# Kernel tuning notes

Hardware: AMD Instinct MI355X
Metric: run time of the kernel (lower is better)

The kernel has to match this reference:

```python
import jax, jax.numpy as jnp
import numpy as np

B, S, H, I, E = 4, 4096, 1024, 4096, 4
VOCAB = 32000


def setup_inputs() -> dict:
    key = jax.random.key(0)
    k1, k2, k3, k4, k5 = jax.random.split(key, 5)
    scale = 1.0 / np.sqrt(H)
    return {
        "hidden_states": jax.random.normal(k1, (B, S, H), dtype=jnp.float32),
        "gate_proj": jax.random.normal(k2, (E, H, I), dtype=jnp.float32) * scale,
        "up_proj": jax.random.normal(k3, (E, H, I), dtype=jnp.float32) * scale,
        "down_proj": jax.random.normal(k4, (E, I, H), dtype=jnp.float32) * (1.0 / np.sqrt(I)),
        "token_ids": jax.random.randint(k5, (B, S), 0, VOCAB, dtype=jnp.int64),
    }


def reference(hidden_states, gate_proj, up_proj, down_proj, token_ids):
    # hidden_states: [B, S, H]; token_ids: [B, S]
    num_experts = gate_proj.shape[0]
    expert_ids = token_ids % num_experts  # [B, S]
    out = jnp.zeros_like(hidden_states)
    for e in range(num_experts):  # small fixed expert loop
        gate = jax.nn.silu(jnp.einsum("bsh,hi->bsi", hidden_states, gate_proj[e]))
        up = jnp.einsum("bsh,hi->bsi", hidden_states, up_proj[e])
        y = jnp.einsum("bsi,ih->bsh", gate * up, down_proj[e])
        out = jnp.where((expert_ids == e)[..., None], y, out)
    return out
```

## Files before the change

### kernel.cpp

```cpp
#include <hip/hip_runtime.h>

#define TOK    16384
#define HD     1024
#define ID     4096
#define NE     4
#define MAXMT  131
#define MAXMT2 67
#define NT32   (HD / 32)

typedef __attribute__((ext_vector_type(4))) float f32x4;
typedef __attribute__((ext_vector_type(8))) short bf16x8;
typedef unsigned int u32;

static __device__ __forceinline__ unsigned short f2bf(float f) {
  unsigned u = __float_as_uint(f);
  u += 0x7FFFu + ((u >> 16) & 1u);
  return (unsigned short)(u >> 16);
}

static __device__ __forceinline__ void gl16(const void* g, void* l) {
  __builtin_amdgcn_global_load_lds((const __attribute__((address_space(1))) u32*)g,
                                   (__attribute__((address_space(3))) u32*)l, 16, 0, 0);
}

static __device__ __forceinline__ void barx() {
  asm volatile("" ::: "memory");
  __builtin_amdgcn_s_barrier();
  asm volatile("" ::: "memory");
}

__global__ void k_route0(const int* __restrict__ ids, int* __restrict__ meta) {
  __shared__ int cnt[4];
  int t = threadIdx.x;
  if (t < 4) cnt[t] = 0;
  __syncthreads();
  int l0 = 0, l1 = 0, l2 = 0, l3 = 0;
  for (int i = t; i < TOK; i += 256) {
    int e = ids[i] & 3;
    l0 += (e == 0); l1 += (e == 1); l2 += (e == 2); l3 += (e == 3);
  }
  atomicAdd(&cnt[0], l0); atomicAdd(&cnt[1], l1);
  atomicAdd(&cnt[2], l2); atomicAdd(&cnt[3], l3);
  __syncthreads();
  if (t == 0) {
    int o = 0;
    for (int e = 0; e < 4; ++e) { meta[e] = o; meta[8 + e] = o; o += cnt[e]; }
    meta[4] = o;
  }
}

__global__ void k_route1(const int* __restrict__ ids, int* __restrict__ meta,
                         int* __restrict__ perm) {
  int i = blockIdx.x * 256 + threadIdx.x;
  if (i < TOK) {
    int e = ids[i] & 3;
    int s = atomicAdd(&meta[8 + e], 1);
    perm[s] = i;
  }
}

__global__ void k_conv(const float* __restrict__ s, unsigned short* __restrict__ d, int n8) {
  int i = blockIdx.x * blockDim.x + threadIdx.x;
  int st = gridDim.x * blockDim.x;
  for (; i < n8; i += st) {
    const f32x4* p = (const f32x4*)(s + ((size_t)i << 3));
    f32x4 a = p[0], b = p[1];
    union { unsigned short u[8]; uint4 q; } o;
    o.u[0] = f2bf(a.x); o.u[1] = f2bf(a.y); o.u[2] = f2bf(a.z); o.u[3] = f2bf(a.w);
    o.u[4] = f2bf(b.x); o.u[5] = f2bf(b.y); o.u[6] = f2bf(b.z); o.u[7] = f2bf(b.w);
    *(uint4*)(d + ((size_t)i << 3)) = o.q;
  }
}

__global__ void k_tr12(const float* __restrict__ gw, const float* __restrict__ uw,
                       const float* __restrict__ dw, unsigned short* __restrict__ gT,
                       unsigned short* __restrict__ uT, unsigned short* __restrict__ dT) {
  __shared__ float tile[64][65];
  int z = blockIdx.y;
  const float* s; unsigned short* d; int R, C, lg;
  if (z < 8) {
    R = HD; C = ID; lg = 6;
    int m = z & 3;
    if (z < 4) { s = gw + (size_t)m * R * C; d = gT + (size_t)m * R * C; }
    else       { s = uw + (size_t)m * R * C; d = uT + (size_t)m * R * C; }
  } else {
    R = ID; C = HD; lg = 4;
    int m = z - 8;
    s = dw + (size_t)m * R * C; d = dT + (size_t)m * R * C;
  }
  int bx = blockIdx.x;
  int tx = bx & ((1 << lg) - 1), ty = bx >> lg;
  int r0 = ty << 6, c0 = tx << 6;
  int t = threadIdx.x;
  int lr = t >> 4, lc = (t & 15) << 2;
  #pragma unroll
  for (int it = 0; it < 4; ++it) {
    int r = lr + (it << 4);
    f32x4 v = *(const f32x4*)(s + (size_t)(r0 + r) * C + c0 + lc);
    tile[r][lc] = v.x; tile[r][lc + 1] = v.y; tile[r][lc + 2] = v.z; tile[r][lc + 3] = v.w;
  }
  __syncthreads();
  int c = t >> 2, rb = (t & 3) << 4;
  union { unsigned short u[16]; uint4 q[2]; } o;
  #pragma unroll
  for (int j = 0; j < 16; ++j) o.u[j] = f2bf(tile[rb + j][c]);
  uint4* dp = (uint4*)(d + (size_t)(c0 + c) * R + r0 + rb);
  dp[0] = o.q[0]; dp[1] = o.q[1];
}

#define MFMA16 __builtin_amdgcn_mfma_f32_16x16x32_bf16
#define BASE4(T) (((T) & 3) * 32768)

#define RD1(T, FA, FB) { const char* bb = smem + BASE4(T); \
  _Pragma("unroll") for (int m = 0; m < 4; ++m) FA[m] = *(const bf16x8*)(bb + offA0[m]); \
  _Pragma("unroll") for (int n = 0; n < 4; ++n) FB[n] = *(const bf16x8*)(bb + offB[n]); }

#define RD2(T, FA) { const char* bb = smem + BASE4(T); \
  _Pragma("unroll") for (int m = 0; m < 4; ++m) FA[m] = *(const bf16x8*)(bb + offA1[m]); }

#define STG(T, H) { int tt = (T) < NT32 ? (T) : NT32 - 1; int ko = tt * 32; \
  char* bb = smem + BASE4(T); \
  gl16(srcA[H] + ko, bb + dA[H]); gl16(srcB[H] + ko, bb + dB[H]); }

#define CLUSTER(FA, FB, MH, NW) \
  barx(); \
  asm volatile("s_waitcnt lgkmcnt(" #NW ")" ::: "memory"); \
  __builtin_amdgcn_sched_barrier(0); \
  __builtin_amdgcn_s_setprio(1); \
  { _Pragma("unroll") for (int m = 0; m < 4; ++m) \
    _Pragma("unroll") for (int n = 0; n < 4; ++n) \
      acc[(MH) * 4 + m][n] = MFMA16(FA[m], FB[n], acc[(MH) * 4 + m][n], 0, 0, 0); } \
  __builtin_amdgcn_s_setprio(0)

__global__ __launch_bounds__(512, 2) void k_gemm1(
    const unsigned short* __restrict__ hid,
    const unsigned short* __restrict__ gT,
    const unsigned short* __restrict__ uT,
    const int* __restrict__ meta,
    const int* __restrict__ perm,
    unsigned short* __restrict__ act) {
  extern __shared__ __align__(16) char smem[];
  int offs[5];
  #pragma unroll
  for (int i = 0; i < 5; ++i) offs[i] = meta[i];
  int bid = blockIdx.x;
  int logical = (bid & 7) * (MAXMT2 * 32 / 8) + (bid >> 3);
  int mt = logical >> 5;
  int ny = logical & 31;
  int e = -1, mloc = 0, base = 0;
  #pragma unroll
  for (int ee = 0; ee < 4; ++ee) {
    int tiles = (offs[ee + 1] - offs[ee] + 255) >> 8;
    if (e < 0 && mt < base + tiles) { e = ee; mloc = mt - base; }
    base += tiles;
  }
  if (e < 0) return;
  int slot0 = offs[e] + (mloc << 8);
  int send = offs[e + 1];
  int tid = threadIdx.x, lane = tid & 63, wid = tid >> 6;
  int n0 = ny << 7;

  int sslot = (tid & 3) ^ ((tid >> 3) & 3);
  int ke = sslot << 3;
  const unsigned short* srcA[2];
  const unsigned short* srcB[2];
  int dA[2], dB[2];
  const unsigned short* gb = gT + (size_t)e * ID * HD;
  const unsigned short* ub = uT + (size_t)e * ID * HD;
  #pragma unroll
  for (int j = 0; j < 2; ++j) {
    int r = (tid >> 2) + j * 128;
    int slot = slot0 + r;
    int pr = perm[slot < send ? slot : slot0];
    srcA[j] = hid + (size_t)pr * HD + ke;
    dA[j] = (tid << 4) + j * 8192;
    int sB = r >> 4;
    int grow = n0 + ((sB >> 1) << 4) + (r & 15);
    srcB[j] = ((sB & 1) ? ub : gb) + (size_t)grow * HD + ke;
    dB[j] = 16384 + (tid << 4) + j * 8192;
  }

  int wm = wid >> 2, wn = wid & 3;
  int r16 = lane & 15, kg = lane >> 4;
  int offA0[4], offA1[4], offB[4];
  #pragma unroll
  for (int m = 0; m < 4; ++m) {
    int r0 = wm * 128 + m * 16 + r16;
    offA0[m] = r0 * 64 + ((kg << 4) ^ (((r0 >> 1) & 3) << 4));
    int r1 = r0 + 64;
    offA1[m] = r1 * 64 + ((kg << 4) ^ (((r1 >> 1) & 3) << 4));
  }
  #pragma unroll
  for (int n = 0; n < 4; ++n) {
    int rb = wn * 64 + n * 16 + r16;
    offB[n] = 16384 + rb * 64 + ((kg << 4) ^ (((rb >> 1) & 3) << 4));
  }

  f32x4 acc[8][4];
  #pragma unroll
  for (int m = 0; m < 8; ++m)
    #pragma unroll
    for (int n = 0; n < 4; ++n) acc[m][n] = (f32x4){0.f, 0.f, 0.f, 0.f};
  bf16x8 faX[4], faY[4], fbE[4], fbO[4];

  STG(0, 0); STG(0, 1);
  STG(1, 0); STG(1, 1);
  STG(2, 0);
  asm volatile("s_waitcnt vmcnt(6)" ::: "memory");
  barx();
  RD1(0, faX, fbE);

  #pragma unroll 1
  for (int i = 0; i < NT32 / 2; ++i) {
    int te = 2 * i, to = 2 * i + 1;
    RD2(te, faY);
    STG(te + 2, 1);
    asm volatile("s_waitcnt vmcnt(4)" ::: "memory");
    CLUSTER(faX, fbE, 0, 4);
    RD1(to, faX, fbO);
    STG(te + 3, 0);
    CLUSTER(faY, fbE, 1, 8);
    RD2(to, faY);
    STG(te + 3, 1);
    asm volatile("s_waitcnt vmcnt(4)" ::: "memory");
    CLUSTER(faX, fbO, 0, 4);
    RD1(te + 2, faX, fbE);
    STG(te + 4, 0);
    CLUSTER(faY, fbO, 1, 8);
  }
  asm volatile("s_waitcnt vmcnt(0) lgkmcnt(0)" ::: "memory");

  #pragma unroll
  for (int mf = 0; mf < 8; ++mf) {
    int lr = wm * 128 + mf * 16 + kg * 4;
    #pragma unroll
    for (int np = 0; np < 2; ++np) {
      int col = n0 + (2 * wn + np) * 16 + r16;
      #pragma unroll
      for (int r = 0; r < 4; ++r) {
        int slot = slot0 + lr + r;
        if (slot < send) {
          float g = acc[mf][2 * np][r];
          float u = acc[mf][2 * np + 1][r];
          float y = (g / (1.f + __expf(-g))) * u;
          act[(size_t)slot * ID + col] = f2bf(y);
        }
      }
    }
  }
}

__global__ __launch_bounds__(256, 2) void k_gemm2(
    const unsigned short* __restrict__ act,
    const unsigned short* __restrict__ dT,
    const int* __restrict__ meta,
    const int* __restrict__ perm,
    float* __restrict__ out) {
  __shared__ unsigned short As[128 * 64];
  __shared__ unsigned short Bs[128 * 64];
  int offs[5];
  #pragma unroll
  for (int i = 0; i < 5; ++i) offs[i] = meta[i];
  int bid = blockIdx.x;
  int logical = (bid & 7) * (MAXMT * 8 / 8) + (bid >> 3);
  int mt = logical >> 3;
  int nyy = logical & 7;
  int e = -1, mloc = 0, base = 0;
  #pragma unroll
  for (int ee = 0; ee < 4; ++ee) {
    int tiles = (offs[ee + 1] - offs[ee] + 127) >> 7;
    if (e < 0 && mt < base + tiles) { e = ee; mloc = mt - base; }
    base += tiles;
  }
  if (e < 0) return;
  int slot0 = offs[e] + (mloc << 7);
  int send = offs[e + 1];
  int tid = threadIdx.x;
  int n0 = nyy << 7;
  const unsigned short* dbase = dT + (size_t)e * HD * ID;
  const unsigned short* ap[4];
  const unsigned short* bp[4];
  int wofs[4];
  #pragma unroll
  for (int it = 0; it < 4; ++it) {
    int b = (tid << 4) + (it << 12);
    int row = b >> 7;
    int kob = b & 127;
    int slot = slot0 + row;
    int s2 = slot < send ? slot : slot0;
    ap[it] = act + (size_t)s2 * ID + (kob >> 1);
    bp[it] = dbase + (size_t)(n0 + row) * ID + (kob >> 1);
    wofs[it] = row * 64 + ((kob ^ ((row & 7) << 4)) >> 1);
  }
  int lane = tid & 63, wid = tid >> 6;
  int wm = wid >> 1, wn = wid & 1;
  int r16 = lane & 15, kg = lane >> 4;
  f32x4 zero = {0.f, 0.f, 0.f, 0.f};
  f32x4 acc[4][4];
  #pragma unroll
  for (int m = 0; m < 4; ++m)
    #pragma unroll
    for (int n = 0; n < 4; ++n) acc[m][n] = zero;

  bf16x8 sa[4], sb[4];
  #pragma unroll
  for (int it = 0; it < 4; ++it) {
    sa[it] = *(const bf16x8*)(ap[it]);
    sb[it] = *(const bf16x8*)(bp[it]);
  }
  for (int kt = 0; kt < ID / 64; ++kt) {
    __syncthreads();
    #pragma unroll
    for (int it = 0; it < 4; ++it) {
      *(bf16x8*)(As + wofs[it]) = sa[it];
      *(bf16x8*)(Bs + wofs[it]) = sb[it];
    }
    __syncthreads();
    if (kt < ID / 64 - 1) {
      int ko = (kt + 1) << 6;
      #pragma unroll
      for (int it = 0; it < 4; ++it) {
        sa[it] = *(const bf16x8*)(ap[it] + ko);
        sb[it] = *(const bf16x8*)(bp[it] + ko);
      }
    }
    #pragma unroll
    for (int kk = 0; kk < 2; ++kk) {
      bf16x8 fa[4], fb[4];
      #pragma unroll
      for (int m = 0; m < 4; ++m) {
        int row = (wm << 6) + (m << 4) + r16;
        int kob = (kk << 6) + (kg << 4);
        fa[m] = *(const bf16x8*)(As + row * 64 + ((kob ^ ((row & 7) << 4)) >> 1));
      }
      #pragma unroll
      for (int n = 0; n < 4; ++n) {
        int row = (wn << 6) + (n << 4) + r16;
        int kob = (kk << 6) + (kg << 4);
        fb[n] = *(const bf16x8*)(Bs + row * 64 + ((kob ^ ((row & 7) << 4)) >> 1));
      }
      #pragma unroll
      for (int m = 0; m < 4; ++m)
        #pragma unroll
        for (int n = 0; n < 4; ++n)
          acc[m][n] = __builtin_amdgcn_mfma_f32_16x16x32_bf16(fa[m], fb[n], acc[m][n], 0, 0, 0);
    }
  }
  #pragma unroll
  for (int m = 0; m < 4; ++m) {
    int lr = (wm << 6) + (m << 4) + (kg << 2);
    int pr4[4];
    #pragma unroll
    for (int r = 0; r < 4; ++r) {
      int slot = slot0 + lr + r;
      pr4[r] = slot < send ? perm[slot] : -1;
    }
    #pragma unroll
    for (int n = 0; n < 4; ++n) {
      int col = n0 + (wn << 6) + (n << 4) + r16;
      #pragma unroll
      for (int r = 0; r < 4; ++r) {
        if (pr4[r] >= 0) out[(size_t)pr4[r] * HD + col] = acc[m][n][r];
      }
    }
  }
}

extern "C" void kernel_launch(void* const* d_in, const int* in_sizes, int n_in,
                              void* d_out, int out_size, void* d_ws, size_t ws_size,
                              hipStream_t stream) {
  const float* hs = (const float*)d_in[0];
  const float* gw = (const float*)d_in[1];
  const float* uw = (const float*)d_in[2];
  const float* dw = (const float*)d_in[3];
  const int* ids = (const int*)d_in[4];
  float* out = (float*)d_out;

  char* w = (char*)d_ws;
  size_t o = 0;
  int* meta = (int*)(w + o); o += 64;
  int* perm = (int*)(w + o); o += (size_t)TOK * 4;
  o = (o + 255) & ~(size_t)255;
  unsigned short* hid = (unsigned short*)(w + o); o += (size_t)TOK * HD * 2;
  unsigned short* gT  = (unsigned short*)(w + o); o += (size_t)NE * ID * HD * 2;
  unsigned short* uT  = (unsigned short*)(w + o); o += (size_t)NE * ID * HD * 2;
  unsigned short* dT  = (unsigned short*)(w + o); o += (size_t)NE * ID * HD * 2;
  unsigned short* actb = (unsigned short*)(w + o); o += (size_t)TOK * ID * 2;

  hipFuncSetAttribute((const void*)k_gemm1,
                      hipFuncAttributeMaxDynamicSharedMemorySize, 131072);

  hipLaunchKernelGGL(k_route0, dim3(1), dim3(256), 0, stream, ids, meta);
  hipLaunchKernelGGL(k_route1, dim3(TOK / 256), dim3(256), 0, stream, ids, meta, perm);
  hipLaunchKernelGGL(k_conv, dim3(2048), dim3(256), 0, stream, hs, hid, TOK * HD / 8);
  hipLaunchKernelGGL(k_tr12, dim3(1024, 12), dim3(256), 0, stream, gw, uw, dw, gT, uT, dT);
  hipLaunchKernelGGL(k_gemm1, dim3(MAXMT2 * 32), dim3(512), 131072, stream,
                     hid, gT, uT, meta, perm, actb);
  hipLaunchKernelGGL(k_gemm2, dim3(MAXMT * 8), dim3(256), 0, stream,
                     actb, dT, meta, perm, out);
}
```

Baseline: 694.0 us.

## Replace pipelined 256-row gemm1 with simpler 128-row single-buffer kernels

Drops the hand-scheduled 4-stage pipelined gemm1 (512 threads, 256x128 tiles, 128KB dynamic LDS) and replaces it with a simple 256-thread kernel on 128-row tiles. The new kernel loads A, gate and up tiles straight to LDS each k-step, waits on vmcnt(0), then runs separate gate and up accumulators. gemm2 is also moved to direct global-to-LDS loads with a swizzled layout, replacing its register-staged copies, and its occupancy hint is raised to 3. The aim is simpler code and higher occupancy, at the cost of losing load/compute overlap and halving M reuse in gemm1.

```diff
diff --git a/kernel.cpp b/kernel.cpp
--- a/kernel.cpp
+++ b/kernel.cpp
@@ -5,8 +5,6 @@
 #define ID     4096
 #define NE     4
 #define MAXMT  131
-#define MAXMT2 67
-#define NT32   (HD / 32)
 
 typedef __attribute__((ext_vector_type(4))) float f32x4;
 typedef __attribute__((ext_vector_type(8))) short bf16x8;
@@ -109,139 +107,119 @@
 }
 
 #define MFMA16 __builtin_amdgcn_mfma_f32_16x16x32_bf16
-#define BASE4(T) (((T) & 3) * 32768)
-
-#define RD1(T, FA, FB) { const char* bb = smem + BASE4(T); \
-  _Pragma("unroll") for (int m = 0; m < 4; ++m) FA[m] = *(const bf16x8*)(bb + offA0[m]); \
-  _Pragma("unroll") for (int n = 0; n < 4; ++n) FB[n] = *(const bf16x8*)(bb + offB[n]); }
-
-#define RD2(T, FA) { const char* bb = smem + BASE4(T); \
-  _Pragma("unroll") for (int m = 0; m < 4; ++m) FA[m] = *(const bf16x8*)(bb + offA1[m]); }
-
-#define STG(T, H) { int tt = (T) < NT32 ? (T) : NT32 - 1; int ko = tt * 32; \
-  char* bb = smem + BASE4(T); \
-  gl16(srcA[H] + ko, bb + dA[H]); gl16(srcB[H] + ko, bb + dB[H]); }
-
-#define CLUSTER(FA, FB, MH, NW) \
-  barx(); \
-  asm volatile("s_waitcnt lgkmcnt(" #NW ")" ::: "memory"); \
-  __builtin_amdgcn_sched_barrier(0); \
-  __builtin_amdgcn_s_setprio(1); \
-  { _Pragma("unroll") for (int m = 0; m < 4; ++m) \
-    _Pragma("unroll") for (int n = 0; n < 4; ++n) \
-      acc[(MH) * 4 + m][n] = MFMA16(FA[m], FB[n], acc[(MH) * 4 + m][n], 0, 0, 0); } \
-  __builtin_amdgcn_s_setprio(0)
-
-__global__ __launch_bounds__(512, 2) void k_gemm1(
+
+__global__ __launch_bounds__(256, 2) void k_gemm1(
     const unsigned short* __restrict__ hid,
     const unsigned short* __restrict__ gT,
     const unsigned short* __restrict__ uT,
     const int* __restrict__ meta,
     const int* __restrict__ perm,
     unsigned short* __restrict__ act) {
-  extern __shared__ __align__(16) char smem[];
+  __shared__ __align__(16) char smem[49152];
   int offs[5];
   #pragma unroll
   for (int i = 0; i < 5; ++i) offs[i] = meta[i];
   int bid = blockIdx.x;
-  int logical = (bid & 7) * (MAXMT2 * 32 / 8) + (bid >> 3);
+  int logical = (bid & 7) * (MAXMT * 32 / 8) + (bid >> 3);
   int mt = logical >> 5;
   int ny = logical & 31;
   int e = -1, mloc = 0, base = 0;
   #pragma unroll
   for (int ee = 0; ee < 4; ++ee) {
-    int tiles = (offs[ee + 1] - offs[ee] + 255) >> 8;
+    int tiles = (offs[ee + 1] - offs[ee] + 127) >> 7;
     if (e < 0 && mt < base + tiles) { e = ee; mloc = mt - base; }
     base += tiles;
   }
   if (e < 0) return;
-  int slot0 = offs[e] + (mloc << 8);
+  int slot0 = offs[e] + (mloc << 7);
   int send = offs[e + 1];
   int tid = threadIdx.x, lane = tid & 63, wid = tid >> 6;
   int n0 = ny << 7;
 
-  int sslot = (tid & 3) ^ ((tid >> 3) & 3);
-  int ke = sslot << 3;
-  const unsigned short* srcA[2];
-  const unsigned short* srcB[2];
-  int dA[2], dB[2];
   const unsigned short* gb = gT + (size_t)e * ID * HD;
   const unsigned short* ub = uT + (size_t)e * ID * HD;
-  #pragma unroll
-  for (int j = 0; j < 2; ++j) {
-    int r = (tid >> 2) + j * 128;
+  int rsub = tid >> 3;
+  int ks = tid & 7;
+  const unsigned short* srcA[4];
+  const unsigned short* srcG[4];
+  const unsigned short* srcU[4];
+  #pragma unroll
+  for (int j = 0; j < 4; ++j) {
+    int r = j * 32 + rsub;
+    int ko = (ks ^ (r & 7)) << 3;
     int slot = slot0 + r;
     int pr = perm[slot < send ? slot : slot0];
-    srcA[j] = hid + (size_t)pr * HD + ke;
-    dA[j] = (tid << 4) + j * 8192;
-    int sB = r >> 4;
-    int grow = n0 + ((sB >> 1) << 4) + (r & 15);
-    srcB[j] = ((sB & 1) ? ub : gb) + (size_t)grow * HD + ke;
-    dB[j] = 16384 + (tid << 4) + j * 8192;
-  }
-
-  int wm = wid >> 2, wn = wid & 3;
+    srcA[j] = hid + (size_t)pr * HD + ko;
+    srcG[j] = gb + (size_t)(n0 + r) * HD + ko;
+    srcU[j] = ub + (size_t)(n0 + r) * HD + ko;
+  }
+  int dstl = tid << 4;
+
+  int wm = wid >> 1, wn = wid & 1;
   int r16 = lane & 15, kg = lane >> 4;
-  int offA0[4], offA1[4], offB[4];
+  int offA[4], offG[4], offU[4];
   #pragma unroll
   for (int m = 0; m < 4; ++m) {
-    int r0 = wm * 128 + m * 16 + r16;
-    offA0[m] = r0 * 64 + ((kg << 4) ^ (((r0 >> 1) & 3) << 4));
-    int r1 = r0 + 64;
-    offA1[m] = r1 * 64 + ((kg << 4) ^ (((r1 >> 1) & 3) << 4));
+    int r = wm * 64 + m * 16 + r16;
+    offA[m] = r * 128 + ((kg ^ (r & 7)) << 4);
   }
   #pragma unroll
   for (int n = 0; n < 4; ++n) {
-    int rb = wn * 64 + n * 16 + r16;
-    offB[n] = 16384 + rb * 64 + ((kg << 4) ^ (((rb >> 1) & 3) << 4));
-  }
-
-  f32x4 acc[8][4];
-  #pragma unroll
-  for (int m = 0; m < 8; ++m)
-    #pragma unroll
-    for (int n = 0; n < 4; ++n) acc[m][n] = (f32x4){0.f, 0.f, 0.f, 0.f};
-  bf16x8 faX[4], faY[4], fbE[4], fbO[4];
-
-  STG(0, 0); STG(0, 1);
-  STG(1, 0); STG(1, 1);
-  STG(2, 0);
-  asm volatile("s_waitcnt vmcnt(6)" ::: "memory");
-  barx();
-  RD1(0, faX, fbE);
-
-  #pragma unroll 1
-  for (int i = 0; i < NT32 / 2; ++i) {
-    int te = 2 * i, to = 2 * i + 1;
-    RD2(te, faY);
-    STG(te + 2, 1);
-    asm volatile("s_waitcnt vmcnt(4)" ::: "memory");
-    CLUSTER(faX, fbE, 0, 4);
-    RD1(to, faX, fbO);
-    STG(te + 3, 0);
-    CLUSTER(faY, fbE, 1, 8);
-    RD2(to, faY);
-    STG(te + 3, 1);
-    asm volatile("s_waitcnt vmcnt(4)" ::: "memory");
-    CLUSTER(faX, fbO, 0, 4);
-    RD1(te + 2, faX, fbE);
-    STG(te + 4, 0);
-    CLUSTER(faY, fbO, 1, 8);
-  }
-  asm volatile("s_waitcnt vmcnt(0) lgkmcnt(0)" ::: "memory");
-
-  #pragma unroll
-  for (int mf = 0; mf < 8; ++mf) {
-    int lr = wm * 128 + mf * 16 + kg * 4;
-    #pragma unroll
-    for (int np = 0; np < 2; ++np) {
-      int col = n0 + (2 * wn + np) * 16 + r16;
+    int r = wn * 64 + n * 16 + r16;
+    int o = r * 128 + ((kg ^ (r & 7)) << 4);
+    offG[n] = 16384 + o;
+    offU[n] = 32768 + o;
+  }
+
+  f32x4 ag[4][4], au[4][4];
+  #pragma unroll
+  for (int m = 0; m < 4; ++m)
+    #pragma unroll
+    for (int n = 0; n < 4; ++n) { ag[m][n] = (f32x4){0,0,0,0}; au[m][n] = (f32x4){0,0,0,0}; }
+
+  for (int t = 0; t < HD / 64; ++t) {
+    barx();
+    int ko = t * 64;
+    #pragma unroll
+    for (int j = 0; j < 4; ++j) gl16(srcA[j] + ko, smem + j * 4096 + dstl);
+    #pragma unroll
+    for (int j = 0; j < 4; ++j) gl16(srcG[j] + ko, smem + 16384 + j * 4096 + dstl);
+    #pragma unroll
+    for (int j = 0; j < 4; ++j) gl16(srcU[j] + ko, smem + 32768 + j * 4096 + dstl);
+    asm volatile("s_waitcnt vmcnt(0)" ::: "memory");
+    barx();
+    #pragma unroll
+    for (int kk = 0; kk < 2; ++kk) {
+      bf16x8 fa[4], fg[4], fu[4];
+      #pragma unroll
+      for (int m = 0; m < 4; ++m) fa[m] = *(const bf16x8*)(smem + (offA[m] ^ (kk << 6)));
+      #pragma unroll
+      for (int n = 0; n < 4; ++n) {
+        fg[n] = *(const bf16x8*)(smem + (offG[n] ^ (kk << 6)));
+        fu[n] = *(const bf16x8*)(smem + (offU[n] ^ (kk << 6)));
+      }
+      #pragma unroll
+      for (int m = 0; m < 4; ++m)
+        #pragma unroll
+        for (int n = 0; n < 4; ++n) {
+          ag[m][n] = MFMA16(fa[m], fg[n], ag[m][n], 0, 0, 0);
+          au[m][n] = MFMA16(fa[m], fu[n], au[m][n], 0, 0, 0);
+        }
+    }
+  }
+
+  #pragma unroll
+  for (int m = 0; m < 4; ++m) {
+    int lr = (wm << 6) + (m << 4) + (kg << 2);
+    #pragma unroll
+    for (int n = 0; n < 4; ++n) {
+      int col = n0 + (wn << 6) + (n << 4) + r16;
       #pragma unroll
       for (int r = 0; r < 4; ++r) {
         int slot = slot0 + lr + r;
         if (slot < send) {
-          float g = acc[mf][2 * np][r];
-          float u = acc[mf][2 * np + 1][r];
+          float g = ag[m][n][r];
+          float u = au[m][n][r];
           float y = (g / (1.f + __expf(-g))) * u;
           act[(size_t)slot * ID + col] = f2bf(y);
         }
@@ -250,14 +228,13 @@
   }
 }
 
-__global__ __launch_bounds__(256, 2) void k_gemm2(
+__global__ __launch_bounds__(256, 3) void k_gemm2(
     const unsigned short* __restrict__ act,
     const unsigned short* __restrict__ dT,
     const int* __restrict__ meta,
     const int* __restrict__ perm,
     float* __restrict__ out) {
-  __shared__ unsigned short As[128 * 64];
-  __shared__ unsigned short Bs[128 * 64];
+  __shared__ __align__(16) char smem[32768];
   int offs[5];
   #pragma unroll
   for (int i = 0; i < 5; ++i) offs[i] = meta[i];
@@ -275,77 +252,69 @@
   if (e < 0) return;
   int slot0 = offs[e] + (mloc << 7);
   int send = offs[e + 1];
-  int tid = threadIdx.x;
+  int tid = threadIdx.x, lane = tid & 63, wid = tid >> 6;
   int n0 = nyy << 7;
   const unsigned short* dbase = dT + (size_t)e * HD * ID;
-  const unsigned short* ap[4];
-  const unsigned short* bp[4];
-  int wofs[4];
-  #pragma unroll
-  for (int it = 0; it < 4; ++it) {
-    int b = (tid << 4) + (it << 12);
-    int row = b >> 7;
-    int kob = b & 127;
-    int slot = slot0 + row;
+
+  int rsub = tid >> 3;
+  int ks = tid & 7;
+  const unsigned short* srcA[4];
+  const unsigned short* srcB[4];
+  #pragma unroll
+  for (int j = 0; j < 4; ++j) {
+    int r = j * 32 + rsub;
+    int ko = (ks ^ (r & 7)) << 3;
+    int slot = slot0 + r;
     int s2 = slot < send ? slot : slot0;
-    ap[it] = act + (size_t)s2 * ID + (kob >> 1);
-    bp[it] = dbase + (size_t)(n0 + row) * ID + (kob >> 1);
-    wofs[it] = row * 64 + ((kob ^ ((row & 7) << 4)) >> 1);
-  }
-  int lane = tid & 63, wid = tid >> 6;
+    srcA[j] = act + (size_t)s2 * ID + ko;
+    srcB[j] = dbase + (size_t)(n0 + r) * ID + ko;
+  }
+  int dstl = tid << 4;
+
   int wm = wid >> 1, wn = wid & 1;
   int r16 = lane & 15, kg = lane >> 4;
-  f32x4 zero = {0.f, 0.f, 0.f, 0.f};
+  int offA[4], offB[4];
+  #pragma unroll
+  for (int m = 0; m < 4; ++m) {
+    int r = wm * 64 + m * 16 + r16;
+    offA[m] = r * 128 + ((kg ^ (r & 7)) << 4);
+  }
+  #pragma unroll
+  for (int n = 0; n < 4; ++n) {
+    int r = wn * 64 + n * 16 + r16;
+    offB[n] = 16384 + r * 128 + ((kg ^ (r & 7)) << 4);
+  }
+
   f32x4 acc[4][4];
   #pragma unroll
   for (int m = 0; m < 4; ++m)
     #pragma unroll
-    for (int n = 0; n < 4; ++n) acc[m][n] = zero;
-
-  bf16x8 sa[4], sb[4];
-  #pragma unroll
-  for (int it = 0; it < 4; ++it) {
-    sa[it] = *(const bf16x8*)(ap[it]);
-    sb[it] = *(const bf16x8*)(bp[it]);
-  }
-  for (int kt = 0; kt < ID / 64; ++kt) {
-    __syncthreads();
-    #pragma unroll
-    for (int it = 0; it < 4; ++it) {
-      *(bf16x8*)(As + wofs[it]) = sa[it];
-      *(bf16x8*)(Bs + wofs[it]) = sb[it];
-    }
-    __syncthreads();
-    if (kt < ID / 64 - 1) {
-      int ko = (kt + 1) << 6;
-      #pragma unroll
-      for (int it = 0; it < 4; ++it) {
-        sa[it] = *(const bf16x8*)(ap[it] + ko);
-        sb[it] = *(const bf16x8*)(bp[it] + ko);
-      }
-    }
+    for (int n = 0; n < 4; ++n) acc[m][n] = (f32x4){0,0,0,0};
+
+  for (int t = 0; t < ID / 64; ++t) {
+    barx();
+    int ko = t * 64;
+    #pragma unroll
+    for (int j = 0; j < 4; ++j) gl16(srcA[j] + ko, smem + j * 4096 + dstl);
+    #pragma unroll
+    for (int j = 0; j < 4; ++j) gl16(srcB[j] + ko, smem + 16384 + j * 4096 + dstl);
+    asm volatile("s_waitcnt vmcnt(0)" ::: "memory");
+    barx();
     #pragma unroll
     for (int kk = 0; kk < 2; ++kk) {
       bf16x8 fa[4], fb[4];
       #pragma unroll
-      for (int m = 0; m < 4; ++m) {
-        int row = (wm << 6) + (m << 4) + r16;
-        int kob = (kk << 6) + (kg << 4);
-        fa[m] = *(const bf16x8*)(As + row * 64 + ((kob ^ ((row & 7) << 4)) >> 1));
-      }
-      #pragma unroll
-      for (int n = 0; n < 4; ++n) {
-        int row = (wn << 6) + (n << 4) + r16;
-        int kob = (kk << 6) + (kg << 4);
-        fb[n] = *(const bf16x8*)(Bs + row * 64 + ((kob ^ ((row & 7) << 4)) >> 1));
-      }
+      for (int m = 0; m < 4; ++m) fa[m] = *(const bf16x8*)(smem + (offA[m] ^ (kk << 6)));
+      #pragma unroll
+      for (int n = 0; n < 4; ++n) fb[n] = *(const bf16x8*)(smem + (offB[n] ^ (kk << 6)));
       #pragma unroll
       for (int m = 0; m < 4; ++m)
         #pragma unroll
         for (int n = 0; n < 4; ++n)
-          acc[m][n] = __builtin_amdgcn_mfma_f32_16x16x32_bf16(fa[m], fb[n], acc[m][n], 0, 0, 0);
-    }
-  }
+          acc[m][n] = MFMA16(fa[m], fb[n], acc[m][n], 0, 0, 0);
+    }
+  }
+
   #pragma unroll
   for (int m = 0; m < 4; ++m) {
     int lr = (wm << 6) + (m << 4) + (kg << 2);
@@ -387,14 +356,11 @@
   unsigned short* dT  = (unsigned short*)(w + o); o += (size_t)NE * ID * HD * 2;
   unsigned short* actb = (unsigned short*)(w + o); o += (size_t)TOK * ID * 2;
 
-  hipFuncSetAttribute((const void*)k_gemm1,
-                      hipFuncAttributeMaxDynamicSharedMemorySize, 131072);
-
   hipLaunchKernelGGL(k_route0, dim3(1), dim3(256), 0, stream, ids, meta);
   hipLaunchKernelGGL(k_route1, dim3(TOK / 256), dim3(256), 0, stream, ids, meta, perm);
   hipLaunchKernelGGL(k_conv, dim3(2048), dim3(256), 0, stream, hs, hid, TOK * HD / 8);
   hipLaunchKernelGGL(k_tr12, dim3(1024, 12), dim3(256), 0, stream, gw, uw, dw, gT, uT, dT);
-  hipLaunchKernelGGL(k_gemm1, dim3(MAXMT2 * 32), dim3(512), 131072, stream,
+  hipLaunchKernelGGL(k_gemm1, dim3(MAXMT * 32), dim3(256), 0, stream,
                      hid, gT, uT, meta, perm, actb);
   hipLaunchKernelGGL(k_gemm2, dim3(MAXMT * 8), dim3(256), 0, stream,
                      actb, dT, meta, perm, out);
```

Result: slower. 714.2 us (+2.9%).
